# Kernel optimization log

Hardware: AMD Instinct MI355X
Metric: run time of the kernel (lower is better)

## Reference

```python
import jax, jax.numpy as jnp
import numpy as np
import math

HIDDEN = 1024
Q_SIZE = 1024
KV_SIZE = 1024
OUT_SIZE = 1024
N_HEADS = 16
D_K = HIDDEN // N_HEADS


def setup_inputs() -> dict:
    key = jax.random.key(0)
    ks = jax.random.split(key, 9)
    b, s, t = 8, 2048, 512
    sc = 0.02
    return {
        "hiddens": jax.random.normal(ks[0], (b, s, KV_SIZE), jnp.float32),
        "query_hiddens": jax.random.normal(ks[1], (b, t, Q_SIZE), jnp.float32),
        "mask": jax.random.randint(ks[2], (b, s), 0, 2, jnp.int32),
        "W_q": jax.random.normal(ks[3], (Q_SIZE, HIDDEN), jnp.float32) * sc,
        "b_q": jnp.zeros((HIDDEN,), jnp.float32),
        "W_k": jax.random.normal(ks[4], (KV_SIZE, HIDDEN), jnp.float32) * sc,
        "W_v": jax.random.normal(ks[5], (KV_SIZE, HIDDEN), jnp.float32) * sc,
        "W_o": jax.random.normal(ks[6], (HIDDEN, OUT_SIZE), jnp.float32) * sc,
        "b_o": jnp.zeros((OUT_SIZE,), jnp.float32),
    }


def reference(hiddens, query_hiddens, mask, W_q, b_q, W_k, W_v, W_o, b_o):
    b, t, _ = query_hiddens.shape
    s = hiddens.shape[1]
    # projections (dropout p=0 in eval -> identity)
    Q = (query_hiddens @ W_q + b_q).reshape(b, t, N_HEADS, D_K)
    K = (hiddens @ W_k).reshape(b, s, N_HEADS, D_K)
    V = (hiddens @ W_v).reshape(b, s, N_HEADS, D_K)
    # scores: [b, t, s, h] matching e = (Q*K).sum(-1)/sqrt(d_k)
    e = jnp.einsum('bthd,bshd->btsh', Q, K) / math.sqrt(D_K)
    neg = (1.0 - mask.astype(e.dtype)) * (-1e20)  # [b, s]
    e = e + neg[:, None, :, None]
    a = jax.nn.softmax(e, axis=2)  # softmax over seqlen
    concat = jnp.einsum('btsh,bshd->bthd', a, V).reshape(b, t, HIDDEN)
    context = concat @ W_o + b_o
    return context, a.mean(axis=-1)
```

## Files before the change

### kernel.cpp

```cpp
#include <hip/hip_runtime.h>
#include <hip/hip_bf16.h>

using short8 = __attribute__((ext_vector_type(8))) short;
using f32x4  = __attribute__((ext_vector_type(4))) float;

#define LSK 72

#define GLDS(gptr, lptr) __builtin_amdgcn_global_load_lds( \
    (const __attribute__((address_space(1))) void*)(gptr), \
    (__attribute__((address_space(3))) void*)(lptr), 16, 0, 0)

static __device__ __forceinline__ short f2b(float f) {
    unsigned u = __builtin_bit_cast(unsigned, f);
    unsigned r = (u + 0x7fffu + ((u >> 16) & 1u)) >> 16;
    return (short)r;
}

__global__ void cvt_bf16(const float* __restrict__ in, short* __restrict__ out, int n) {
    int i = (blockIdx.x * 256 + threadIdx.x) * 4;
    if (i >= n) return;
    float4 v = *(const float4*)(in + i);
    short4 o = make_short4(f2b(v.x), f2b(v.y), f2b(v.z), f2b(v.w));
    *(short4*)(out + i) = o;
}

__global__ void cvt_t4(const float* __restrict__ W0, const float* __restrict__ W1,
                       const float* __restrict__ W2, const float* __restrict__ W3,
                       short* __restrict__ Wt0) {
    __shared__ short tile[32][33];
    const float* Ws[4] = {W0, W1, W2, W3};
    const float* W = Ws[blockIdx.z];
    short* Wt = Wt0 + (size_t)blockIdx.z * 1024 * 1024;
    const int K = 1024, N = 1024;
    int n0 = blockIdx.x * 32, k0 = blockIdx.y * 32;
    int tx = threadIdx.x, ty = threadIdx.y;
#pragma unroll
    for (int i = 0; i < 4; i++) {
        int r = ty + i * 8;
        tile[r][tx] = f2b(W[(size_t)(k0 + r) * N + n0 + tx]);
    }
    __syncthreads();
#pragma unroll
    for (int i = 0; i < 4; i++) {
        int r = ty + i * 8;
        Wt[(size_t)(n0 + r) * K + k0 + tx] = tile[tx][r];
    }
}

__global__ __launch_bounds__(256) void gemm128(
    const short* __restrict__ A, const short* __restrict__ Bt,
    const float* __restrict__ bias, void* __restrict__ Cout, void* __restrict__ Cout2,
    int M, int mode)
{
    __shared__ short As[128 * 64];
    __shared__ short Bs[128 * 64];
    const int tid = threadIdx.x;
    const int w = tid >> 6, L = tid & 63, quad = L >> 4, l16 = L & 15;
    const int wr = w >> 1, wc = w & 1;

    const int lin = blockIdx.y * gridDim.x + blockIdx.x;
    const int xcd = lin & 7, idx = lin >> 3;
    const int mPer = gridDim.y >> 3;
    const int my = xcd * mPer + idx / gridDim.x;
    const int nx = idx % gridDim.x;
    const int n0 = nx * 128, m0 = my * 128;

    const int K = 1024;
    const int srow_in = L >> 3;
    const int sgcol   = ((L & 7) ^ (srow_in & 7)) * 8;

    f32x4 acc[4][4];
#pragma unroll
    for (int mi = 0; mi < 4; mi++)
#pragma unroll
        for (int ni = 0; ni < 4; ni++) acc[mi][ni] = (f32x4){0.f, 0.f, 0.f, 0.f};

    for (int k0 = 0; k0 < K; k0 += 64) {
#pragma unroll
        for (int j = 0; j < 8; j++) {
            int c = w * 8 + j;
            if (c < 16) {
                int row = c * 8 + srow_in;
                GLDS(A + (size_t)(m0 + row) * K + k0 + sgcol, &As[c * 512]);
            } else {
                int row = (c - 16) * 8 + srow_in;
                GLDS(Bt + (size_t)(n0 + row) * K + k0 + sgcol, &Bs[(c - 16) * 512]);
            }
        }
        __syncthreads();
#pragma unroll
        for (int kk = 0; kk < 64; kk += 32) {
            const int swz = (((kk >> 3) + quad) ^ (l16 & 7)) << 3;
            short8 af[4], bf[4];
#pragma unroll
            for (int mi = 0; mi < 4; mi++)
                af[mi] = *(const short8*)&As[(wr * 64 + mi * 16 + l16) * 64 + swz];
#pragma unroll
            for (int ni = 0; ni < 4; ni++)
                bf[ni] = *(const short8*)&Bs[(wc * 64 + ni * 16 + l16) * 64 + swz];
#pragma unroll
            for (int mi = 0; mi < 4; mi++)
#pragma unroll
                for (int ni = 0; ni < 4; ni++)
                    acc[mi][ni] = __builtin_amdgcn_mfma_f32_16x16x32_bf16(af[mi], bf[ni], acc[mi][ni], 0, 0, 0);
        }
        __syncthreads();
    }
#pragma unroll
    for (int ni = 0; ni < 4; ni++) {
        int n = n0 + wc * 64 + ni * 16 + l16;
        float bv = (mode != 2 && bias) ? bias[n] : 0.f;
#pragma unroll
    for (int mi = 0; mi < 4; mi++) {
#pragma unroll
            for (int r = 0; r < 4; r++) {
                int m = m0 + wr * 64 + mi * 16 + quad * 4 + r;
                float v = acc[mi][ni][r] + bv;
                if (mode == 1)      ((float*)Cout)[(size_t)m * 1024 + n] = v;
                else if (mode == 0) ((short*)Cout)[(size_t)m * 1024 + n] = f2b(v);
                else {
                    if (n < 1024) ((short*)Cout)[(size_t)m * 1024 + n] = f2b(v);
                    else {
                        int h = (n - 1024) >> 6, d = n & 63;
                        int b = m >> 11, s = m & 2047;
                        ((short*)Cout2)[(((size_t)b * 16 + h) * 64 + d) * 2048 + s] = f2b(v);
                    }
                }
            }
        }
    }
}

__global__ __launch_bounds__(512) void attn_flash(
    const short* __restrict__ Qb, const short* __restrict__ Kb, const short* __restrict__ Vtb,
    const int* __restrict__ mask, short* __restrict__ Cb, float* __restrict__ lse)
{
    __shared__ short Qs[128 * 64];
    __shared__ short Ks[128 * 64];
    __shared__ short Vts[128 * 64];
    __shared__ short Ps[128 * LSK];
    __shared__ float neg[128];
    const int tid = threadIdx.x;
    const int w = tid >> 6, L = tid & 63, quad = L >> 4, l16 = L & 15;
    const int t0 = blockIdx.x * 128, h = blockIdx.y, b = blockIdx.z;
    const int S = 2048, T = 512, H = 1024;
    const int trow = w * 16;
    const int srow = L >> 3;
    const int sg   = ((L & 7) ^ srow) * 8;

#pragma unroll
    for (int j = 0; j < 2; j++) {
        int row = w * 16 + j * 8 + srow;
        GLDS(Qb + ((size_t)b * T + t0 + row) * H + h * 64 + sg, &Qs[(w * 16 + j * 8) * 64]);
    }
    __syncthreads();
    short8 aq[2];
#pragma unroll
    for (int kk = 0; kk < 2; kk++)
        aq[kk] = *(const short8*)&Qs[(trow + l16) * 64 + ((kk * 4 + quad) ^ (l16 & 7)) * 8];

    f32x4 Oacc[4];
#pragma unroll
    for (int nt = 0; nt < 4; nt++) Oacc[nt] = (f32x4){0.f, 0.f, 0.f, 0.f};
    float lsum[4] = {0.f, 0.f, 0.f, 0.f};

    for (int s0 = 0; s0 < S; s0 += 128) {
#pragma unroll
        for (int j = 0; j < 2; j++) {
            int krow = w * 16 + j * 8 + srow;
            GLDS(Kb + ((size_t)b * S + s0 + krow) * H + h * 64 + sg, &Ks[(w * 16 + j * 8) * 64]);
            int c = w * 2 + j, hf = c >> 3, d0 = (c & 7) * 8;
            GLDS(Vtb + (((size_t)b * 16 + h) * 64 + d0 + srow) * S + s0 + hf * 64 + sg, &Vts[c * 512]);
        }
        if (tid < 128) neg[tid] = mask[(size_t)b * S + s0 + tid] ? 0.f : -1e20f;
        __syncthreads();
#pragma unroll
        for (int hf = 0; hf < 2; hf++) {
            f32x4 sacc[4];
#pragma unroll
            for (int nt = 0; nt < 4; nt++) sacc[nt] = (f32x4){0.f, 0.f, 0.f, 0.f};
#pragma unroll
            for (int kk = 0; kk < 2; kk++) {
#pragma unroll
                for (int nt = 0; nt < 4; nt++) {
                    short8 bf = *(const short8*)&Ks[(hf * 64 + nt * 16 + l16) * 64 + ((kk * 4 + quad) ^ (l16 & 7)) * 8];
                    sacc[nt] = __builtin_amdgcn_mfma_f32_16x16x32_bf16(aq[kk], bf, sacc[nt], 0, 0, 0);
                }
            }
#pragma unroll
            for (int nt = 0; nt < 4; nt++) {
                float ng = neg[hf * 64 + nt * 16 + l16];
#pragma unroll
                for (int r = 0; r < 4; r++) {
                    float e = __expf(fmaf(sacc[nt][r], 0.125f, ng));
                    lsum[r] += e;
                    Ps[(trow + quad * 4 + r) * LSK + nt * 16 + l16] = f2b(e);
                }
            }
#pragma unroll
            for (int kk = 0; kk < 2; kk++) {
                short8 af = *(const short8*)&Ps[(trow + l16) * LSK + kk * 32 + quad * 8];
#pragma unroll
                for (int nt = 0; nt < 4; nt++) {
                    short8 bf = *(const short8*)&Vts[hf * 4096 + (nt * 16 + l16) * 64 + ((kk * 4 + quad) ^ (l16 & 7)) * 8];
                    Oacc[nt] = __builtin_amdgcn_mfma_f32_16x16x32_bf16(af, bf, Oacc[nt], 0, 0, 0);
                }
            }
        }
        __syncthreads();
    }
#pragma unroll
    for (int r = 0; r < 4; r++) {
#pragma unroll
        for (int off = 1; off < 16; off <<= 1)
            lsum[r] += __shfl_xor(lsum[r], off, 64);
    }
#pragma unroll
    for (int r = 0; r < 4; r++) {
        float inv = 1.0f / lsum[r];
        int t = t0 + trow + quad * 4 + r;
#pragma unroll
        for (int nt = 0; nt < 4; nt++) {
            int d = nt * 16 + l16;
            Cb[((size_t)b * T + t) * H + h * 64 + d] = f2b(Oacc[nt][r] * inv);
        }
        if (l16 == 0)
            lse[((size_t)b * 16 + h) * T + t] = __logf(lsum[r]);
    }
}

__global__ __launch_bounds__(256) void attn_amean(
    const short* __restrict__ Qb, const short* __restrict__ Kb,
    const int* __restrict__ mask, const float* __restrict__ lse, float* __restrict__ outA)
{
    __shared__ short Qs[64 * 64];
    __shared__ short Ks[64 * 64];
    __shared__ float neg[64];
    __shared__ float lss[16 * 64];
    const int tid = threadIdx.x;
    const int w = tid >> 6, L = tid & 63, quad = L >> 4, l16 = L & 15;
    const int s0 = blockIdx.x * 64, t0 = blockIdx.y * 64, b = blockIdx.z;
    const int S = 2048, T = 512, H = 1024;
    const int srow = L >> 3;
    const int sg   = ((L & 7) ^ srow) * 8;

    if (tid < 64) neg[tid] = mask[(size_t)b * S + s0 + tid] ? 0.f : -1e20f;
    for (int i = tid; i < 16 * 64; i += 256) {
        int hh = i >> 6, tt = i & 63;
        lss[i] = lse[((size_t)b * 16 + hh) * T + t0 + tt];
    }
    float am[4][4] = {};
    for (int h = 0; h < 16; h++) {
        __syncthreads();
#pragma unroll
        for (int j = 0; j < 2; j++) {
            int row = w * 16 + j * 8 + srow;
            GLDS(Qb + ((size_t)b * T + t0 + row) * H + h * 64 + sg, &Qs[(w * 16 + j * 8) * 64]);
            GLDS(Kb + ((size_t)b * S + s0 + row) * H + h * 64 + sg, &Ks[(w * 16 + j * 8) * 64]);
        }
        __syncthreads();
        short8 aq[2];
#pragma unroll
        for (int kk = 0; kk < 2; kk++)
            aq[kk] = *(const short8*)&Qs[(w * 16 + l16) * 64 + ((kk * 4 + quad) ^ (l16 & 7)) * 8];
        f32x4 sacc[4];
#pragma unroll
        for (int nt = 0; nt < 4; nt++) sacc[nt] = (f32x4){0.f, 0.f, 0.f, 0.f};
#pragma unroll
        for (int kk = 0; kk < 2; kk++) {
#pragma unroll
            for (int nt = 0; nt < 4; nt++) {
                short8 bf = *(const short8*)&Ks[(nt * 16 + l16) * 64 + ((kk * 4 + quad) ^ (l16 & 7)) * 8];
                sacc[nt] = __builtin_amdgcn_mfma_f32_16x16x32_bf16(aq[kk], bf, sacc[nt], 0, 0, 0);
            }
        }
#pragma unroll
        for (int nt = 0; nt < 4; nt++) {
            float ng = neg[nt * 16 + l16];
#pragma unroll
            for (int r = 0; r < 4; r++) {
                int trow = w * 16 + quad * 4 + r;
                am[nt][r] += __expf(fmaf(sacc[nt][r], 0.125f, ng - lss[h * 64 + trow]));
            }
        }
    }
#pragma unroll
    for (int r = 0; r < 4; r++) {
        int t = t0 + w * 16 + quad * 4 + r;
#pragma unroll
        for (int nt = 0; nt < 4; nt++) {
            int s = s0 + nt * 16 + l16;
            outA[((size_t)b * T + t) * S + s] = am[nt][r] * 0.0625f;
        }
    }
}

extern "C" void kernel_launch(void* const* d_in, const int* in_sizes, int n_in,
                              void* d_out, int out_size, void* d_ws, size_t ws_size,
                              hipStream_t stream) {
    const float* hiddens = (const float*)d_in[0];
    const float* query   = (const float*)d_in[1];
    const int*   mask    = (const int*)d_in[2];
    const float* W_q = (const float*)d_in[3];
    const float* b_q = (const float*)d_in[4];
    const float* W_k = (const float*)d_in[5];
    const float* W_v = (const float*)d_in[6];
    const float* W_o = (const float*)d_in[7];
    const float* b_o = (const float*)d_in[8];
    float* out = (float*)d_out;

    constexpr size_t N_H  = 8UL * 2048 * 1024;
    constexpr size_t N_QH = 8UL * 512 * 1024;
    constexpr size_t N_W  = 1024UL * 1024;
    char* ws = (char*)d_ws;
    short* Hb   = (short*)(ws);
    short* QHb  = (short*)(ws + N_H * 2);
    short* Wqt  = (short*)(ws + N_H * 2 + N_QH * 2);
    short* Wkt  = Wqt + N_W;
    short* Wvt  = Wkt + N_W;
    short* Wot  = Wvt + N_W;
    short* Qb   = Wot + N_W;
    short* Kb   = Qb + N_QH;
    short* Vtb  = Kb + N_H;
    short* Cb   = Vtb + N_H;
    float* lseP = (float*)(Cb + N_QH);

    cvt_bf16<<<16384, 256, 0, stream>>>(hiddens, Hb, (int)N_H);
    cvt_bf16<<<4096, 256, 0, stream>>>(query, QHb, (int)N_QH);
    cvt_t4<<<dim3(32, 32, 4), dim3(32, 8), 0, stream>>>(W_q, W_k, W_v, W_o, Wqt);

    gemm128<<<dim3(8, 32), 256, 0, stream>>>(QHb, Wqt, b_q, Qb, nullptr, 4096, 0);
    gemm128<<<dim3(16, 128), 256, 0, stream>>>(Hb, Wkt, nullptr, Kb, Vtb, 16384, 2);

    attn_flash<<<dim3(4, 16, 8), 512, 0, stream>>>(Qb, Kb, Vtb, mask, Cb, lseP);

    gemm128<<<dim3(8, 32), 256, 0, stream>>>(Cb, Wot, b_o, out, nullptr, 4096, 1);
    attn_amean<<<dim3(32, 8, 8), 256, 0, stream>>>(Qb, Kb, mask, lseP, out + N_QH);
}
```

Measured before the change: 427.1 us.

## Double-buffer LDS tiles in GEMM, flash attention and amean kernels

Adds ping-pong LDS buffers to the projection GEMM, flash attention and attention-mean kernels. The next K-tile, KV tile or head's Q/K tile is issued with global_load_lds before the current tile is computed, and each iteration now needs only one barrier. This is meant to hide global-to-LDS latency behind MFMA work. The cost is roughly doubled LDS use per block, which can lower occupancy, especially for the 512-thread flash kernel. The barrier's wait for outstanding loads may also limit how much overlap is gained.

```diff
diff --git a/kernel.cpp b/kernel.cpp
--- a/kernel.cpp
+++ b/kernel.cpp
@@ -52,8 +52,8 @@
     const float* __restrict__ bias, void* __restrict__ Cout, void* __restrict__ Cout2,
     int M, int mode)
 {
-    __shared__ short As[128 * 64];
-    __shared__ short Bs[128 * 64];
+    __shared__ short As[2][128 * 64];
+    __shared__ short Bs[2][128 * 64];
     const int tid = threadIdx.x;
     const int w = tid >> 6, L = tid & 63, quad = L >> 4, l16 = L & 15;
     const int wr = w >> 1, wc = w & 1;
@@ -69,35 +69,42 @@
     const int srow_in = L >> 3;
     const int sgcol   = ((L & 7) ^ (srow_in & 7)) * 8;
 
-    f32x4 acc[4][4];
-#pragma unroll
-    for (int mi = 0; mi < 4; mi++)
-#pragma unroll
-        for (int ni = 0; ni < 4; ni++) acc[mi][ni] = (f32x4){0.f, 0.f, 0.f, 0.f};
-
-    for (int k0 = 0; k0 < K; k0 += 64) {
+    auto STAGE = [&](int buf, int k0) {
 #pragma unroll
         for (int j = 0; j < 8; j++) {
             int c = w * 8 + j;
             if (c < 16) {
                 int row = c * 8 + srow_in;
-                GLDS(A + (size_t)(m0 + row) * K + k0 + sgcol, &As[c * 512]);
+                GLDS(A + (size_t)(m0 + row) * K + k0 + sgcol, &As[buf][c * 512]);
             } else {
                 int row = (c - 16) * 8 + srow_in;
-                GLDS(Bt + (size_t)(n0 + row) * K + k0 + sgcol, &Bs[(c - 16) * 512]);
-            }
-        }
-        __syncthreads();
+                GLDS(Bt + (size_t)(n0 + row) * K + k0 + sgcol, &Bs[buf][(c - 16) * 512]);
+            }
+        }
+    };
+
+    f32x4 acc[4][4];
+#pragma unroll
+    for (int mi = 0; mi < 4; mi++)
+#pragma unroll
+        for (int ni = 0; ni < 4; ni++) acc[mi][ni] = (f32x4){0.f, 0.f, 0.f, 0.f};
+
+    STAGE(0, 0);
+    __syncthreads();
+
+    for (int t = 0; t < 16; t++) {
+        const int cur = t & 1;
+        if (t < 15) STAGE(cur ^ 1, (t + 1) * 64);
 #pragma unroll
         for (int kk = 0; kk < 64; kk += 32) {
             const int swz = (((kk >> 3) + quad) ^ (l16 & 7)) << 3;
             short8 af[4], bf[4];
 #pragma unroll
             for (int mi = 0; mi < 4; mi++)
-                af[mi] = *(const short8*)&As[(wr * 64 + mi * 16 + l16) * 64 + swz];
+                af[mi] = *(const short8*)&As[cur][(wr * 64 + mi * 16 + l16) * 64 + swz];
 #pragma unroll
             for (int ni = 0; ni < 4; ni++)
-                bf[ni] = *(const short8*)&Bs[(wc * 64 + ni * 16 + l16) * 64 + swz];
+                bf[ni] = *(const short8*)&Bs[cur][(wc * 64 + ni * 16 + l16) * 64 + swz];
 #pragma unroll
             for (int mi = 0; mi < 4; mi++)
 #pragma unroll
@@ -106,12 +113,13 @@
         }
         __syncthreads();
     }
+
 #pragma unroll
     for (int ni = 0; ni < 4; ni++) {
         int n = n0 + wc * 64 + ni * 16 + l16;
         float bv = (mode != 2 && bias) ? bias[n] : 0.f;
 #pragma unroll
-    for (int mi = 0; mi < 4; mi++) {
+        for (int mi = 0; mi < 4; mi++) {
 #pragma unroll
             for (int r = 0; r < 4; r++) {
                 int m = m0 + wr * 64 + mi * 16 + quad * 4 + r;
@@ -136,10 +144,10 @@
     const int* __restrict__ mask, short* __restrict__ Cb, float* __restrict__ lse)
 {
     __shared__ short Qs[128 * 64];
-    __shared__ short Ks[128 * 64];
-    __shared__ short Vts[128 * 64];
+    __shared__ short Ks[2][128 * 64];
+    __shared__ short Vts[2][128 * 64];
     __shared__ short Ps[128 * LSK];
-    __shared__ float neg[128];
+    __shared__ float neg[2][128];
     const int tid = threadIdx.x;
     const int w = tid >> 6, L = tid & 63, quad = L >> 4, l16 = L & 15;
     const int t0 = blockIdx.x * 128, h = blockIdx.y, b = blockIdx.z;
@@ -148,12 +156,25 @@
     const int srow = L >> 3;
     const int sg   = ((L & 7) ^ srow) * 8;
 
+    auto STAGE_KV = [&](int buf, int s0) {
+#pragma unroll
+        for (int j = 0; j < 2; j++) {
+            int krow = w * 16 + j * 8 + srow;
+            GLDS(Kb + ((size_t)b * S + s0 + krow) * H + h * 64 + sg, &Ks[buf][(w * 16 + j * 8) * 64]);
+            int c = w * 2 + j, hf = c >> 3, d0 = (c & 7) * 8;
+            GLDS(Vtb + (((size_t)b * 16 + h) * 64 + d0 + srow) * S + s0 + hf * 64 + sg, &Vts[buf][c * 512]);
+        }
+        if (tid < 128) neg[buf][tid] = mask[(size_t)b * S + s0 + tid] ? 0.f : -1e20f;
+    };
+
 #pragma unroll
     for (int j = 0; j < 2; j++) {
         int row = w * 16 + j * 8 + srow;
         GLDS(Qb + ((size_t)b * T + t0 + row) * H + h * 64 + sg, &Qs[(w * 16 + j * 8) * 64]);
     }
+    STAGE_KV(0, 0);
     __syncthreads();
+
     short8 aq[2];
 #pragma unroll
     for (int kk = 0; kk < 2; kk++)
@@ -164,16 +185,9 @@
     for (int nt = 0; nt < 4; nt++) Oacc[nt] = (f32x4){0.f, 0.f, 0.f, 0.f};
     float lsum[4] = {0.f, 0.f, 0.f, 0.f};
 
-    for (int s0 = 0; s0 < S; s0 += 128) {
-#pragma unroll
-        for (int j = 0; j < 2; j++) {
-            int krow = w * 16 + j * 8 + srow;
-            GLDS(Kb + ((size_t)b * S + s0 + krow) * H + h * 64 + sg, &Ks[(w * 16 + j * 8) * 64]);
-            int c = w * 2 + j, hf = c >> 3, d0 = (c & 7) * 8;
-            GLDS(Vtb + (((size_t)b * 16 + h) * 64 + d0 + srow) * S + s0 + hf * 64 + sg, &Vts[c * 512]);
-        }
-        if (tid < 128) neg[tid] = mask[(size_t)b * S + s0 + tid] ? 0.f : -1e20f;
-        __syncthreads();
+    for (int it = 0; it < 16; it++) {
+        const int cur = it & 1;
+        if (it < 15) STAGE_KV(cur ^ 1, (it + 1) * 128);
 #pragma unroll
         for (int hf = 0; hf < 2; hf++) {
             f32x4 sacc[4];
@@ -183,13 +197,13 @@
             for (int kk = 0; kk < 2; kk++) {
 #pragma unroll
                 for (int nt = 0; nt < 4; nt++) {
-                    short8 bf = *(const short8*)&Ks[(hf * 64 + nt * 16 + l16) * 64 + ((kk * 4 + quad) ^ (l16 & 7)) * 8];
+                    short8 bf = *(const short8*)&Ks[cur][(hf * 64 + nt * 16 + l16) * 64 + ((kk * 4 + quad) ^ (l16 & 7)) * 8];
                     sacc[nt] = __builtin_amdgcn_mfma_f32_16x16x32_bf16(aq[kk], bf, sacc[nt], 0, 0, 0);
                 }
             }
 #pragma unroll
             for (int nt = 0; nt < 4; nt++) {
-                float ng = neg[hf * 64 + nt * 16 + l16];
+                float ng = neg[cur][hf * 64 + nt * 16 + l16];
 #pragma unroll
                 for (int r = 0; r < 4; r++) {
                     float e = __expf(fmaf(sacc[nt][r], 0.125f, ng));
@@ -202,7 +216,7 @@
                 short8 af = *(const short8*)&Ps[(trow + l16) * LSK + kk * 32 + quad * 8];
 #pragma unroll
                 for (int nt = 0; nt < 4; nt++) {
-                    short8 bf = *(const short8*)&Vts[hf * 4096 + (nt * 16 + l16) * 64 + ((kk * 4 + quad) ^ (l16 & 7)) * 8];
+                    short8 bf = *(const short8*)&Vts[cur][hf * 4096 + (nt * 16 + l16) * 64 + ((kk * 4 + quad) ^ (l16 & 7)) * 8];
                     Oacc[nt] = __builtin_amdgcn_mfma_f32_16x16x32_bf16(af, bf, Oacc[nt], 0, 0, 0);
                 }
             }
@@ -233,8 +247,8 @@
     const short* __restrict__ Qb, const short* __restrict__ Kb,
     const int* __restrict__ mask, const float* __restrict__ lse, float* __restrict__ outA)
 {
-    __shared__ short Qs[64 * 64];
-    __shared__ short Ks[64 * 64];
+    __shared__ short Qs[2][64 * 64];
+    __shared__ short Ks[2][64 * 64];
     __shared__ float neg[64];
     __shared__ float lss[16 * 64];
     const int tid = threadIdx.x;
@@ -244,25 +258,31 @@
     const int srow = L >> 3;
     const int sg   = ((L & 7) ^ srow) * 8;
 
+    auto STAGE_QK = [&](int buf, int h) {
+#pragma unroll
+        for (int j = 0; j < 2; j++) {
+            int row = w * 16 + j * 8 + srow;
+            GLDS(Qb + ((size_t)b * T + t0 + row) * H + h * 64 + sg, &Qs[buf][(w * 16 + j * 8) * 64]);
+            GLDS(Kb + ((size_t)b * S + s0 + row) * H + h * 64 + sg, &Ks[buf][(w * 16 + j * 8) * 64]);
+        }
+    };
+
     if (tid < 64) neg[tid] = mask[(size_t)b * S + s0 + tid] ? 0.f : -1e20f;
     for (int i = tid; i < 16 * 64; i += 256) {
         int hh = i >> 6, tt = i & 63;
         lss[i] = lse[((size_t)b * 16 + hh) * T + t0 + tt];
     }
+    STAGE_QK(0, 0);
+    __syncthreads();
+
     float am[4][4] = {};
     for (int h = 0; h < 16; h++) {
-        __syncthreads();
-#pragma unroll
-        for (int j = 0; j < 2; j++) {
-            int row = w * 16 + j * 8 + srow;
-            GLDS(Qb + ((size_t)b * T + t0 + row) * H + h * 64 + sg, &Qs[(w * 16 + j * 8) * 64]);
-            GLDS(Kb + ((size_t)b * S + s0 + row) * H + h * 64 + sg, &Ks[(w * 16 + j * 8) * 64]);
-        }
-        __syncthreads();
+        const int cur = h & 1;
+        if (h < 15) STAGE_QK(cur ^ 1, h + 1);
         short8 aq[2];
 #pragma unroll
         for (int kk = 0; kk < 2; kk++)
-            aq[kk] = *(const short8*)&Qs[(w * 16 + l16) * 64 + ((kk * 4 + quad) ^ (l16 & 7)) * 8];
+            aq[kk] = *(const short8*)&Qs[cur][(w * 16 + l16) * 64 + ((kk * 4 + quad) ^ (l16 & 7)) * 8];
         f32x4 sacc[4];
 #pragma unroll
         for (int nt = 0; nt < 4; nt++) sacc[nt] = (f32x4){0.f, 0.f, 0.f, 0.f};
@@ -270,7 +290,7 @@
         for (int kk = 0; kk < 2; kk++) {
 #pragma unroll
             for (int nt = 0; nt < 4; nt++) {
-                short8 bf = *(const short8*)&Ks[(nt * 16 + l16) * 64 + ((kk * 4 + quad) ^ (l16 & 7)) * 8];
+                short8 bf = *(const short8*)&Ks[cur][(nt * 16 + l16) * 64 + ((kk * 4 + quad) ^ (l16 & 7)) * 8];
                 sacc[nt] = __builtin_amdgcn_mfma_f32_16x16x32_bf16(aq[kk], bf, sacc[nt], 0, 0, 0);
             }
         }
@@ -283,6 +303,7 @@
                 am[nt][r] += __expf(fmaf(sacc[nt][r], 0.125f, ng - lss[h * 64 + trow]));
             }
         }
+        __syncthreads();
     }
 #pragma unroll
     for (int r = 0; r < 4; r++) {
```

Result: no change. 433.2 us (+1.4%).
